# Performance work log

Hardware: AMD Instinct MI355X
Metric: run time of the kernel (lower is better)

Reference implementation:

```python
import jax, jax.numpy as jnp
import numpy as np

NUM_LAYERS = 32
NUM_SLOTS = 128
HIDDEN = 4096
T_WRITE = 128   # == NUM_SLOTS so slot_ids form a permutation (deterministic scatter)
T_READ = 8192
EMA_ALPHA = 0.1


def setup_inputs() -> dict:
    key = jax.random.key(0)
    ks = jax.random.split(key, 4)
    values = jax.random.normal(ks[0], (T_WRITE, HIDDEN), jnp.float32)
    queries = jax.random.normal(ks[1], (T_READ, HIDDEN), jnp.float32)
    memory = jax.random.normal(ks[2], (NUM_LAYERS, NUM_SLOTS, HIDDEN), jnp.float32) * 0.02
    gate_w = jax.random.normal(ks[3], (NUM_LAYERS, HIDDEN), jnp.float32) * (1.0 / np.sqrt(HIDDEN))
    gate_b = jnp.zeros((NUM_LAYERS,), jnp.float32)
    return {
        "values": values,
        "queries": queries,
        "memory": memory,
        "gate_w": gate_w,
        "gate_b": gate_b,
        "layer_idx": 0,
        "k": 8,
        "ptr": 0,
    }


def reference(values, queries, memory, gate_w, gate_b, layer_idx, k, ptr):
    # ---- write(): EMA scatter into one layer's slots ----
    mem_l = memory[layer_idx]                                  # [N, d]
    g = jax.nn.sigmoid(values @ gate_w[layer_idx] + gate_b[layer_idx])[:, None]  # [T,1]
    T = values.shape[0]
    slot_ids = (ptr + jnp.arange(T)) % NUM_SLOTS               # [T]
    current = mem_l[slot_ids]                                  # gather [T, d]
    updated = EMA_ALPHA * g * values + (1.0 - EMA_ALPHA) * current
    mem_new = mem_l.at[slot_ids].set(updated)                  # scatter-write [N, d]

    # ---- read(): matmul -> top-k -> gather -> softmax -> weighted sum ----
    scale = 1.0 / jnp.sqrt(jnp.float32(HIDDEN))
    scores = (queries @ mem_new.T) * scale                     # [T_read, N]
    topk_scores, topk_idx = jax.lax.top_k(scores, k)           # [T_read, k]
    attn = jax.nn.softmax(topk_scores, axis=-1)                # [T_read, k]
    topk_v = mem_new[topk_idx]                                 # gather [T_read, k, d]
    out = jnp.einsum('tk,tkd->td', attn, topk_v)               # [T_read, d]
    return out
```

## Files before the change

### kernel.cpp

```cpp
#include <hip/hip_runtime.h>
#include <math.h>

#define D 4096
#define NSLOTS 128
#define TR 8192
#define NKQ 8
#define KCH 512
#define EPS_TRIG 1e-3f
#define WIN 5e-4f

typedef __attribute__((ext_vector_type(8))) short bf16x8;
typedef __attribute__((ext_vector_type(4))) float f32x4;

union BV { bf16x8 v; unsigned u[4]; };

__device__ __forceinline__ unsigned short bfrne(float x) {
  unsigned u = __float_as_uint(x);
  unsigned r = u + 0x7fffu + ((u >> 16) & 1u);
  return (unsigned short)(r >> 16);
}

__device__ __forceinline__ void gload16(const void* gsrc, void* ldst) {
  __builtin_amdgcn_global_load_lds(
      (const __attribute__((address_space(1))) void*)gsrc,
      (__attribute__((address_space(3))) void*)ldst, 16, 0, 0);
}

__global__ __launch_bounds__(256) void update_mem_kernel(
    const float* __restrict__ values, const float* __restrict__ memory,
    const float* __restrict__ gate_w, const float* __restrict__ gate_b,
    const int* __restrict__ layer_idx_p, const int* __restrict__ ptr_p,
    int T_W, float* __restrict__ ws_mem,
    unsigned short* __restrict__ MFh,
    unsigned short* __restrict__ Mth, unsigned short* __restrict__ Mtm) {
  const int l = layer_idx_p[0], p = ptr_p[0], s = blockIdx.x, tid = threadIdx.x;
  int t0 = ((s - p) % NSLOTS + NSLOTS) % NSLOTS;
  const bool written = (t0 < T_W);
  const int t = written ? (t0 + ((T_W - 1 - t0) / NSLOTS) * NSLOTS) : 0;
  const float* mrow = memory + ((size_t)l * NSLOTS + s) * D;
  const float* vrow = values + (size_t)t * D;

  float acoef = 0.f, bcoef = 1.0f;
  if (written) {
    const float* gw = gate_w + (size_t)l * D;
    double acc = 0.0;
    for (int j = tid; j < D; j += 256)
      acc += (double)vrow[j] * (double)gw[j];
    for (int off = 32; off; off >>= 1) acc += __shfl_down(acc, off, 64);
    __shared__ double wsum[4];
    if ((tid & 63) == 0) wsum[tid >> 6] = acc;
    __syncthreads();
    double dot = wsum[0] + wsum[1] + wsum[2] + wsum[3];
    float x = (float)dot + gate_b[l];
    float g = 1.0f / (1.0f + expf(-x));
    acoef = 0.1f * g; bcoef = 0.9f;
  }

  const int sg = s >> 4, fr = s & 15;
  for (int j8 = tid; j8 < D / 8; j8 += 256) {
    float4 mv0 = ((const float4*)mrow)[j8 * 2];
    float4 mv1 = ((const float4*)mrow)[j8 * 2 + 1];
    float4 vv0 = make_float4(0.f, 0.f, 0.f, 0.f), vv1 = vv0;
    if (written) {
      vv0 = ((const float4*)vrow)[j8 * 2];
      vv1 = ((const float4*)vrow)[j8 * 2 + 1];
    }
    float ov[8];
    ov[0] = acoef * vv0.x + bcoef * mv0.x;
    ov[1] = acoef * vv0.y + bcoef * mv0.y;
    ov[2] = acoef * vv0.z + bcoef * mv0.z;
    ov[3] = acoef * vv0.w + bcoef * mv0.w;
    ov[4] = acoef * vv1.x + bcoef * mv1.x;
    ov[5] = acoef * vv1.y + bcoef * mv1.y;
    ov[6] = acoef * vv1.z + bcoef * mv1.z;
    ov[7] = acoef * vv1.w + bcoef * mv1.w;
    ((float4*)(ws_mem + (size_t)s * D))[j8 * 2] =
        make_float4(ov[0], ov[1], ov[2], ov[3]);
    ((float4*)(ws_mem + (size_t)s * D))[j8 * 2 + 1] =
        make_float4(ov[4], ov[5], ov[6], ov[7]);

    unsigned short h[8], md[8];
#pragma unroll
    for (int e = 0; e < 8; ++e) {
      h[e] = bfrne(ov[e]);
      float f = __uint_as_float((unsigned)h[e] << 16);
      md[e] = bfrne(ov[e] - f);
    }
    const int ks = j8 >> 2, fo = j8 & 3;
    const size_t unit = (size_t)ks * 512 + sg * 64 + fo * 16 + fr;
    uint4 hp;
    hp.x = (unsigned)h[0] | ((unsigned)h[1] << 16);
    hp.y = (unsigned)h[2] | ((unsigned)h[3] << 16);
    hp.z = (unsigned)h[4] | ((unsigned)h[5] << 16);
    hp.w = (unsigned)h[6] | ((unsigned)h[7] << 16);
    ((uint4*)MFh)[unit] = hp;
#pragma unroll
    for (int e = 0; e < 8; ++e) {
      Mth[(size_t)(j8 * 8 + e) * NSLOTS + s] = h[e];
      Mtm[(size_t)(j8 * 8 + e) * NSLOTS + s] = md[e];
    }
  }
}

__global__ __launch_bounds__(256) void scores_kernel(
    const float* __restrict__ queries, const unsigned short* __restrict__ MFh,
    float* __restrict__ part) {
  __shared__ float Qs[2][4096];

  const int tid = threadIdx.x, lane = tid & 63, w = tid >> 6;
  const int fr = lane & 15, fo = lane >> 4;
  const int qt = blockIdx.x >> 3, kq = blockIdx.x & (NKQ - 1);
  const int qbase = qt * 128;
  const int kbase = kq * KCH;

  const int rl = lane >> 3, ul = lane & 7;
  const int su = ul ^ rl;
  const float* qsrc[4];
#pragma unroll
  for (int i = 0; i < 4; ++i) {
    int g = w * 4 + i;
    qsrc[i] = queries + (size_t)(qbase + 8 * g + rl) * D + kbase + su * 4;
  }

  const unsigned short* bh_base = MFh + (size_t)lane * 8;
  const size_t kqoff = (size_t)kq * 16 * 512 * 8;

  f32x4 acc[2][8];
#pragma unroll
  for (int rg = 0; rg < 2; ++rg)
#pragma unroll
    for (int cg = 0; cg < 8; ++cg) acc[rg][cg] = (f32x4){0.f, 0.f, 0.f, 0.f};

#define STG(B, S) do {                                                       \
    const int k0_ = (S) * 32;                                                \
    _Pragma("unroll")                                                        \
    for (int i = 0; i < 4; ++i)                                              \
      gload16(qsrc[i] + k0_, &Qs[B][(w * 4 + i) * 256]);                     \
  } while (0)

#define CMP(B, S) do {                                                       \
    const size_t soff = kqoff + (size_t)(S) * 512 * 8;                       \
    bf16x8 bh_[8];                                                           \
    _Pragma("unroll")                                                        \
    for (int cg = 0; cg < 8; ++cg)                                           \
      bh_[cg] = *(const bf16x8*)(bh_base + soff + cg * 64 * 8);              \
    _Pragma("unroll")                                                        \
    for (int rg = 0; rg < 2; ++rg) {                                         \
      const int row = w * 32 + rg * 16 + fr;                                 \
      float4 a0 = *(const float4*)&Qs[B][row * 32 + (((fo * 2) ^ (row & 7)) << 2)]; \
      float4 a1 = *(const float4*)&Qs[B][row * 32 + ((((fo * 2) | 1) ^ (row & 7)) << 2)]; \
      float qf[8] = {a0.x, a0.y, a0.z, a0.w, a1.x, a1.y, a1.z, a1.w};        \
      BV ah;                                                                 \
      _Pragma("unroll")                                                      \
      for (int i = 0; i < 4; ++i) {                                          \
        unsigned u0 = __float_as_uint(qf[2 * i]);                            \
        unsigned u1 = __float_as_uint(qf[2 * i + 1]);                        \
        ah.u[i] = (u0 >> 16) | (u1 & 0xffff0000u);         \
      }                                                                      \
      _Pragma("unroll")                                                      \
      for (int cg = 0; cg < 8; ++cg)                                         \
        acc[rg][cg] = __builtin_amdgcn_mfma_f32_16x16x32_bf16(ah.v, bh_[cg], acc[rg][cg], 0, 0, 0); \
    }                                                                        \
  } while (0)

  STG(0, 0);
  __syncthreads();
  for (int s = 0; s < 16; ++s) {
    const int cur = s & 1;
    if (s < 15) STG(cur ^ 1, s + 1);
    CMP(cur, s);
    __syncthreads();
  }
#undef STG
#undef CMP

  float* op = part + ((size_t)kq * TR + qbase) * NSLOTS;
#pragma unroll
  for (int rg = 0; rg < 2; ++rg)
#pragma unroll
    for (int cg = 0; cg < 8; ++cg)
#pragma unroll
      for (int r = 0; r < 4; ++r)
        op[(size_t)(w * 32 + rg * 16 + fo * 4 + r) * NSLOTS + cg * 16 + fr] =
            acc[rg][cg][r];
}

__device__ __forceinline__ unsigned mapf(float f) {
  unsigned u = __float_as_uint(f);
  return (u & 0x80000000u) ? ~u : (u | 0x80000000u);
}
__device__ __forceinline__ float unmapf(unsigned u) {
  return __uint_as_float((u & 0x80000000u) ? (u & 0x7fffffffu) : ~u);
}

__device__ __forceinline__ void wave_select(
    float va, float vb, int l, int k, int iters,
    float &m, float &sum, bool &sela, bool &selb, float &vkm1, float &vkk) {
  m = 0.f; sum = 0.f; sela = false; selb = false; vkm1 = 0.f; vkk = -3.4e38f;
  for (int it = 0; it < iters; ++it) {
    unsigned long long ka =
        ((unsigned long long)mapf(va) << 32) | (unsigned)(127 - l);
    unsigned long long kb =
        ((unsigned long long)mapf(vb) << 32) | (unsigned)(63 - l);
    unsigned long long key = ka > kb ? ka : kb;
#pragma unroll
    for (int off = 32; off; off >>= 1) {
      unsigned long long o = __shfl_xor(key, off, 64);
      if (o > key) key = o;
    }
    int idx = 127 - (int)(unsigned)(key & 0xffffffffULL);
    float val = unmapf((unsigned)(key >> 32));
    if (it == 0) m = val;
    if (it < k) sum += expf(val - m);
    if (it == k - 1) vkm1 = val;
    if (it == k) vkk = val;
    if (idx == l) { sela = sela || (it < k); va = -INFINITY; }
    if (idx == l + 64) { selb = selb || (it < k); vb = -INFINITY; }
  }
}

__device__ __forceinline__ float rescore_slot(const float* __restrict__ qrow,
                                              const float* __restrict__ mrow,
                                              int l) {
  double acc = 0.0;
#pragma unroll 4
  for (int c = 0; c < 16; ++c) {
    int j = c * 256 + l * 4;
    float4 qv = *(const float4*)(qrow + j);
    float4 mv = *(const float4*)(mrow + j);
    acc += (double)qv.x * (double)mv.x;
    acc += (double)qv.y * (double)mv.y;
    acc += (double)qv.z * (double)mv.z;
    acc += (double)qv.w * (double)mv.w;
  }
#pragma unroll
  for (int off = 32; off; off >>= 1) acc += __shfl_xor(acc, off, 64);
  return (float)(acc * 0.015625);
}

__global__ __launch_bounds__(256) void topk_kernel(
    const float* __restrict__ part, const float* __restrict__ ws_mem,
    const float* __restrict__ queries, const int* __restrict__ k_p,
    unsigned short* __restrict__ Ah, unsigned short* __restrict__ Am) {
  const int w = threadIdx.x >> 6, l = threadIdx.x & 63;
  const int row = blockIdx.x * 4 + w;
  int k = k_p[0];
  if (k < 1) k = 1;
  if (k > NSLOTS) k = NSLOTS;
  const int ksel = (k < NSLOTS) ? k + 1 : k;

  float origa = 0.f, origb = 0.f;
#pragma unroll
  for (int kq = 0; kq < NKQ; ++kq) {
    origa += part[((size_t)kq * TR + row) * NSLOTS + l];
    origb += part[((size_t)kq * TR + row) * NSLOTS + 64 + l];
  }
  origa *= 0.015625f;
  origb *= 0.015625f;

  float m, sum, vkm1, vkk;
  bool sela, selb;
  wave_select(origa, origb, l, k, ksel, m, sum, sela, selb, vkm1, vkk);

  if (ksel > k && (vkm1 - vkk) < EPS_TRIG) {
    const float* qrow = queries + (size_t)row * D;
    float lo = vkk - WIN, hi = vkm1 + WIN;
    unsigned long long ba = __ballot(origa >= lo && origa <= hi);
    unsigned long long bb = __ballot(origb >= lo && origb <= hi);
    while (ba) {
      int s = __ffsll(ba) - 1; ba &= ba - 1;
      float ex = rescore_slot(qrow, ws_mem + (size_t)s * D, l);
      if (l == s) origa = ex;
    }
    while (bb) {
      int s = __ffsll(bb) - 1; bb &= bb - 1;
      float ex = rescore_slot(qrow, ws_mem + (size_t)(s + 64) * D, l);
      if (l == s) origb = ex;
    }
    wave_select(origa, origb, l, k, k, m, sum, sela, selb, vkm1, vkk);
  }

  const float inv = 1.0f / sum;
  float wa = sela ? expf(origa - m) * inv : 0.f;
  float wb = selb ? expf(origb - m) * inv : 0.f;

  unsigned short ha = bfrne(wa);
  unsigned short ma = bfrne(wa - __uint_as_float((unsigned)ha << 16));
  unsigned short hb = bfrne(wb);
  unsigned short mb = bfrne(wb - __uint_as_float((unsigned)hb << 16));
  Ah[(size_t)row * NSLOTS + l] = ha;
  Am[(size_t)row * NSLOTS + l] = ma;
  Ah[(size_t)row * NSLOTS + 64 + l] = hb;
  Am[(size_t)row * NSLOTS + 64 + l] = mb;
}

__global__ __launch_bounds__(256) void gather_kernel(
    const unsigned short* __restrict__ Ah, const unsigned short* __restrict__ Am,
    const unsigned short* __restrict__ Mth, const unsigned short* __restrict__ Mtm,
    float* __restrict__ out) {
  __shared__ char lds[65536];
  const int tid = threadIdx.x, lane = tid & 63, w = tid >> 6;
  const int fr = lane & 15, fo = lane >> 4;
  const int rowblk = blockIdx.x >> 6, colblk = blockIdx.x & 63;
  const int r0 = rowblk * 64, c0 = colblk * 64;

  const unsigned short* srcbase =
      (w == 0) ? Ah + (size_t)r0 * NSLOTS :
      (w == 1) ? Am + (size_t)r0 * NSLOTS :
      (w == 2) ? Mth + (size_t)c0 * NSLOTS :
                 Mtm + (size_t)c0 * NSLOTS;
#pragma unroll
  for (int i = 0; i < 16; ++i) {
    int dl = i * 64 + lane;
    int row = dl >> 4, u = dl & 15;
    int su = u ^ (row & 7);
    gload16(srcbase + (size_t)row * NSLOTS + su * 8,
            lds + w * 16384 + i * 1024);
  }
  __syncthreads();

  const int rw = w >> 1, cw = w & 1;
  f32x4 acc[2][2];
#pragma unroll
  for (int rg = 0; rg < 2; ++rg)
#pragma unroll
    for (int cg = 0; cg < 2; ++cg) acc[rg][cg] = (f32x4){0.f, 0.f, 0.f, 0.f};

#pragma unroll
  for (int c = 0; c < 4; ++c) {
    bf16x8 ah_[2], am_[2], bh_[2], bm_[2];
#pragma unroll
    for (int rg = 0; rg < 2; ++rg) {
      int row = rw * 32 + rg * 16 + fr;
      int off = row * 256 + ((c * 64 + fo * 16) ^ ((row & 7) << 4));
      ah_[rg] = *(const bf16x8*)(lds + off);
      am_[rg] = *(const bf16x8*)(lds + 16384 + off);
    }
#pragma unroll
    for (int cg = 0; cg < 2; ++cg) {
      int col = cw * 32 + cg * 16 + fr;
      int off = col * 256 + ((c * 64 + fo * 16) ^ ((col & 7) << 4));
      bh_[cg] = *(const bf16x8*)(lds + 32768 + off);
      bm_[cg] = *(const bf16x8*)(lds + 49152 + off);
    }
#pragma unroll
    for (int rg = 0; rg < 2; ++rg)
#pragma unroll
      for (int cg = 0; cg < 2; ++cg) {
        acc[rg][cg] = __builtin_amdgcn_mfma_f32_16x16x32_bf16(am_[rg], bh_[cg], acc[rg][cg], 0, 0, 0);
        acc[rg][cg] = __builtin_amdgcn_mfma_f32_16x16x32_bf16(ah_[rg], bm_[cg], acc[rg][cg], 0, 0, 0);
        acc[rg][cg] = __builtin_amdgcn_mfma_f32_16x16x32_bf16(ah_[rg], bh_[cg], acc[rg][cg], 0, 0, 0);
      }
  }
  __syncthreads();

  float* O = (float*)lds;
#pragma unroll
  for (int rg = 0; rg < 2; ++rg)
#pragma unroll
    for (int cg = 0; cg < 2; ++cg)
#pragma unroll
      for (int r = 0; r < 4; ++r)
        O[(rw * 32 + rg * 16 + fo * 4 + r) * 132 + cw * 32 + cg * 16 + fr] =
            acc[rg][cg][r];
  __syncthreads();

#pragma unroll
  for (int i = 0; i < 4; ++i) {
    int idx = tid + i * 256;
    int row = idx >> 4, c4 = idx & 15;
    float4 v = *(const float4*)(O + row * 132 + c4 * 4);
    *(float4*)(out + (size_t)(r0 + row) * D + c0 + c4 * 4) = v;
  }
}

extern "C" void kernel_launch(void* const* d_in, const int* in_sizes, int n_in,
                              void* d_out, int out_size, void* d_ws, size_t ws_size,
                              hipStream_t stream) {
  const float* values  = (const float*)d_in[0];
  const float* queries = (const float*)d_in[1];
  const float* memory  = (const float*)d_in[2];
  const float* gate_w  = (const float*)d_in[3];
  const float* gate_b  = (const float*)d_in[4];
  const int* layer_idx = (const int*)d_in[5];
  const int* k_p       = (const int*)d_in[6];
  const int* ptr_p     = (const int*)d_in[7];

  const int T_W = in_sizes[0] / D;
  const int T_R = in_sizes[1] / D;

  float* ws_mem = (float*)d_ws;
  float* part   = ws_mem + (size_t)NSLOTS * D;
  unsigned short* MFh = (unsigned short*)(part + (size_t)NKQ * TR * NSLOTS);
  unsigned short* Mth = MFh + (size_t)NSLOTS * D;
  unsigned short* Mtm = Mth + (size_t)NSLOTS * D;
  unsigned short* Ah  = Mtm + (size_t)NSLOTS * D;
  unsigned short* Am  = Ah  + (size_t)T_R * NSLOTS;

  update_mem_kernel<<<NSLOTS, 256, 0, stream>>>(
      values, memory, gate_w, gate_b, layer_idx, ptr_p, T_W,
      ws_mem, MFh, Mth, Mtm);
  scores_kernel<<<(T_R / 128) * NKQ, 256, 0, stream>>>(queries, MFh, part);
  topk_kernel<<<T_R / 4, 256, 0, stream>>>(part, ws_mem, queries, k_p, Ah, Am);
  gather_kernel<<<(T_R / 64) * (D / 64), 256, 0, stream>>>(Ah, Am, Mth, Mtm,
                                                           (float*)d_out);
}
```

Before: 139.0 us.

## Pre-swizzle attention and memory operands into MFMA fragment layout, drop LDS staging

The topk and update kernels now write the bf16 hi/lo attention weights and transposed memory directly in MFMA fragment order. The gather kernel can then load operands straight from global memory into registers, with no LDS staging or barriers. The gather tile grows to 128x128 per block: each wave keeps its A fragments in registers and streams B fragments across 8 column groups. Output is stored directly from accumulators without an LDS transpose, which makes the stores less coalesced (16 columns per row). The scattered 2-byte writes in the producer kernels also add cost.

After: 132.8 us. -4.5%, faster.

```diff
diff --git a/kernel.cpp b/kernel.cpp
--- a/kernel.cpp
+++ b/kernel.cpp
@@ -32,7 +32,7 @@
     const int* __restrict__ layer_idx_p, const int* __restrict__ ptr_p,
     int T_W, float* __restrict__ ws_mem,
     unsigned short* __restrict__ MFh,
-    unsigned short* __restrict__ Mth, unsigned short* __restrict__ Mtm) {
+    unsigned short* __restrict__ BTFh, unsigned short* __restrict__ BTFm) {
   const int l = layer_idx_p[0], p = ptr_p[0], s = blockIdx.x, tid = threadIdx.x;
   int t0 = ((s - p) % NSLOTS + NSLOTS) % NSLOTS;
   const bool written = (t0 < T_W);
@@ -56,7 +56,8 @@
     acoef = 0.1f * g; bcoef = 0.9f;
   }
 
-  const int sg = s >> 4, fr = s & 15;
+  const int sg = s >> 4, fr_s = s & 15;
+  const int ksS = s >> 5, foS = (s >> 3) & 3, posS = s & 7;
   for (int j8 = tid; j8 < D / 8; j8 += 256) {
     float4 mv0 = ((const float4*)mrow)[j8 * 2];
     float4 mv1 = ((const float4*)mrow)[j8 * 2 + 1];
@@ -87,7 +88,7 @@
       md[e] = bfrne(ov[e] - f);
     }
     const int ks = j8 >> 2, fo = j8 & 3;
-    const size_t unit = (size_t)ks * 512 + sg * 64 + fo * 16 + fr;
+    const size_t unit = (size_t)ks * 512 + sg * 64 + fo * 16 + fr_s;
     uint4 hp;
     hp.x = (unsigned)h[0] | ((unsigned)h[1] << 16);
     hp.y = (unsigned)h[2] | ((unsigned)h[3] << 16);
@@ -96,8 +97,10 @@
     ((uint4*)MFh)[unit] = hp;
 #pragma unroll
     for (int e = 0; e < 8; ++e) {
-      Mth[(size_t)(j8 * 8 + e) * NSLOTS + s] = h[e];
-      Mtm[(size_t)(j8 * 8 + e) * NSLOTS + s] = md[e];
+      int c = j8 * 8 + e;
+      size_t u = ((size_t)(c >> 4) * 4 + ksS) * 64 + foS * 16 + (c & 15);
+      BTFh[u * 8 + posS] = h[e];
+      BTFm[u * 8 + posS] = md[e];
     }
   }
 }
@@ -241,7 +244,7 @@
 __global__ __launch_bounds__(256) void topk_kernel(
     const float* __restrict__ part, const float* __restrict__ ws_mem,
     const float* __restrict__ queries, const int* __restrict__ k_p,
-    unsigned short* __restrict__ Ah, unsigned short* __restrict__ Am) {
+    unsigned short* __restrict__ AFh, unsigned short* __restrict__ AFm) {
   const int w = threadIdx.x >> 6, l = threadIdx.x & 63;
   const int row = blockIdx.x * 4 + w;
   int k = k_p[0];
@@ -288,89 +291,60 @@
   unsigned short ma = bfrne(wa - __uint_as_float((unsigned)ha << 16));
   unsigned short hb = bfrne(wb);
   unsigned short mb = bfrne(wb - __uint_as_float((unsigned)hb << 16));
-  Ah[(size_t)row * NSLOTS + l] = ha;
-  Am[(size_t)row * NSLOTS + l] = ma;
-  Ah[(size_t)row * NSLOTS + 64 + l] = hb;
-  Am[(size_t)row * NSLOTS + 64 + l] = mb;
+
+  const int rg = row >> 4, frr = row & 15;
+  const size_t ua =
+      (((size_t)rg * 4 + (l >> 5)) * 64 + ((l >> 3) & 3) * 16 + frr) * 8 + (l & 7);
+  const size_t ub =
+      (((size_t)rg * 4 + (l >> 5) + 2) * 64 + ((l >> 3) & 3) * 16 + frr) * 8 + (l & 7);
+  AFh[ua] = ha; AFm[ua] = ma;
+  AFh[ub] = hb; AFm[ub] = mb;
 }
 
 __global__ __launch_bounds__(256) void gather_kernel(
-    const unsigned short* __restrict__ Ah, const unsigned short* __restrict__ Am,
-    const unsigned short* __restrict__ Mth, const unsigned short* __restrict__ Mtm,
+    const unsigned short* __restrict__ AFh, const unsigned short* __restrict__ AFm,
+    const unsigned short* __restrict__ BTFh, const unsigned short* __restrict__ BTFm,
     float* __restrict__ out) {
-  __shared__ char lds[65536];
   const int tid = threadIdx.x, lane = tid & 63, w = tid >> 6;
   const int fr = lane & 15, fo = lane >> 4;
-  const int rowblk = blockIdx.x >> 6, colblk = blockIdx.x & 63;
-  const int r0 = rowblk * 64, c0 = colblk * 64;
-
-  const unsigned short* srcbase =
-      (w == 0) ? Ah + (size_t)r0 * NSLOTS :
-      (w == 1) ? Am + (size_t)r0 * NSLOTS :
-      (w == 2) ? Mth + (size_t)c0 * NSLOTS :
-                 Mtm + (size_t)c0 * NSLOTS;
-#pragma unroll
-  for (int i = 0; i < 16; ++i) {
-    int dl = i * 64 + lane;
-    int row = dl >> 4, u = dl & 15;
-    int su = u ^ (row & 7);
-    gload16(srcbase + (size_t)row * NSLOTS + su * 8,
-            lds + w * 16384 + i * 1024);
-  }
-  __syncthreads();
-
-  const int rw = w >> 1, cw = w & 1;
-  f32x4 acc[2][2];
+  const int rowblk = blockIdx.x >> 5, colblk = blockIdx.x & 31;
+  const int r0 = rowblk * 128 + w * 32;
+  const int rg0 = r0 >> 4;
+
+  bf16x8 a_h[2][4], a_m[2][4];
 #pragma unroll
   for (int rg = 0; rg < 2; ++rg)
 #pragma unroll
-    for (int cg = 0; cg < 2; ++cg) acc[rg][cg] = (f32x4){0.f, 0.f, 0.f, 0.f};
-
-#pragma unroll
-  for (int c = 0; c < 4; ++c) {
-    bf16x8 ah_[2], am_[2], bh_[2], bm_[2];
+    for (int ks = 0; ks < 4; ++ks) {
+      const size_t u = (((size_t)(rg0 + rg) * 4 + ks) * 64 + lane) * 8;
+      a_h[rg][ks] = *(const bf16x8*)(AFh + u);
+      a_m[rg][ks] = *(const bf16x8*)(AFm + u);
+    }
+
+#pragma unroll 2
+  for (int cgi = 0; cgi < 8; ++cgi) {
+    const int cg = colblk * 8 + cgi;
+    bf16x8 b_h[4], b_m[4];
+#pragma unroll
+    for (int ks = 0; ks < 4; ++ks) {
+      const size_t u = (((size_t)cg * 4 + ks) * 64 + lane) * 8;
+      b_h[ks] = *(const bf16x8*)(BTFh + u);
+      b_m[ks] = *(const bf16x8*)(BTFm + u);
+    }
+    const int col = cg * 16 + fr;
 #pragma unroll
     for (int rg = 0; rg < 2; ++rg) {
-      int row = rw * 32 + rg * 16 + fr;
-      int off = row * 256 + ((c * 64 + fo * 16) ^ ((row & 7) << 4));
-      ah_[rg] = *(const bf16x8*)(lds + off);
-      am_[rg] = *(const bf16x8*)(lds + 16384 + off);
-    }
-#pragma unroll
-    for (int cg = 0; cg < 2; ++cg) {
-      int col = cw * 32 + cg * 16 + fr;
-      int off = col * 256 + ((c * 64 + fo * 16) ^ ((col & 7) << 4));
-      bh_[cg] = *(const bf16x8*)(lds + 32768 + off);
-      bm_[cg] = *(const bf16x8*)(lds + 49152 + off);
-    }
-#pragma unroll
-    for (int rg = 0; rg < 2; ++rg)
-#pragma unroll
-      for (int cg = 0; cg < 2; ++cg) {
-        acc[rg][cg] = __builtin_amdgcn_mfma_f32_16x16x32_bf16(am_[rg], bh_[cg], acc[rg][cg], 0, 0, 0);
-        acc[rg][cg] = __builtin_amdgcn_mfma_f32_16x16x32_bf16(ah_[rg], bm_[cg], acc[rg][cg], 0, 0, 0);
-        acc[rg][cg] = __builtin_amdgcn_mfma_f32_16x16x32_bf16(ah_[rg], bh_[cg], acc[rg][cg], 0, 0, 0);
+      f32x4 acc = {0.f, 0.f, 0.f, 0.f};
+#pragma unroll
+      for (int ks = 0; ks < 4; ++ks) {
+        acc = __builtin_amdgcn_mfma_f32_16x16x32_bf16(a_m[rg][ks], b_h[ks], acc, 0, 0, 0);
+        acc = __builtin_amdgcn_mfma_f32_16x16x32_bf16(a_h[rg][ks], b_m[ks], acc, 0, 0, 0);
+        acc = __builtin_amdgcn_mfma_f32_16x16x32_bf16(a_h[rg][ks], b_h[ks], acc, 0, 0, 0);
       }
-  }
-  __syncthreads();
-
-  float* O = (float*)lds;
-#pragma unroll
-  for (int rg = 0; rg < 2; ++rg)
-#pragma unroll
-    for (int cg = 0; cg < 2; ++cg)
 #pragma unroll
       for (int r = 0; r < 4; ++r)
-        O[(rw * 32 + rg * 16 + fo * 4 + r) * 132 + cw * 32 + cg * 16 + fr] =
-            acc[rg][cg][r];
-  __syncthreads();
-
-#pragma unroll
-  for (int i = 0; i < 4; ++i) {
-    int idx = tid + i * 256;
-    int row = idx >> 4, c4 = idx & 15;
-    float4 v = *(const float4*)(O + row * 132 + c4 * 4);
-    *(float4*)(out + (size_t)(r0 + row) * D + c0 + c4 * 4) = v;
+        out[(size_t)(r0 + rg * 16 + fo * 4 + r) * D + col] = acc[r];
+    }
   }
 }
 
@@ -391,17 +365,17 @@
 
   float* ws_mem = (float*)d_ws;
   float* part   = ws_mem + (size_t)NSLOTS * D;
-  unsigned short* MFh = (unsigned short*)(part + (size_t)NKQ * TR * NSLOTS);
-  unsigned short* Mth = MFh + (size_t)NSLOTS * D;
-  unsigned short* Mtm = Mth + (size_t)NSLOTS * D;
-  unsigned short* Ah  = Mtm + (size_t)NSLOTS * D;
-  unsigned short* Am  = Ah  + (size_t)T_R * NSLOTS;
+  unsigned short* MFh  = (unsigned short*)(part + (size_t)NKQ * TR * NSLOTS);
+  unsigned short* BTFh = MFh  + (size_t)NSLOTS * D;
+  unsigned short* BTFm = BTFh + (size_t)NSLOTS * D;
+  unsigned short* AFh  = BTFm + (size_t)NSLOTS * D;
+  unsigned short* AFm  = AFh  + (size_t)T_R * NSLOTS;
 
   update_mem_kernel<<<NSLOTS, 256, 0, stream>>>(
       values, memory, gate_w, gate_b, layer_idx, ptr_p, T_W,
-      ws_mem, MFh, Mth, Mtm);
+      ws_mem, MFh, BTFh, BTFm);
   scores_kernel<<<(T_R / 128) * NKQ, 256, 0, stream>>>(queries, MFh, part);
-  topk_kernel<<<T_R / 4, 256, 0, stream>>>(part, ws_mem, queries, k_p, Ah, Am);
-  gather_kernel<<<(T_R / 64) * (D / 64), 256, 0, stream>>>(Ah, Am, Mth, Mtm,
-                                                           (float*)d_out);
-}
+  topk_kernel<<<T_R / 4, 256, 0, stream>>>(part, ws_mem, queries, k_p, AFh, AFm);
+  gather_kernel<<<(T_R / 128) * (D / 128), 256, 0, stream>>>(AFh, AFm, BTFh, BTFm,
+                                                             (float*)d_out);
+}
```
